# Performance work log

Hardware: AMD Instinct MI355X
Metric: run time of the kernel (lower is better)

Reference implementation:

```python
import jax, jax.numpy as jnp
import numpy as np

HEADS = 16
DIM_HEAD = 64
SCALE = DIM_HEAD ** -0.5


def setup_inputs() -> dict:
    key = jax.random.key(0)
    ks = jax.random.split(key, 6)
    d = 1024
    x = jax.random.normal(ks[0], (4, 2048, d), dtype=jnp.float32)
    s = d ** -0.5
    Wq = jax.random.normal(ks[1], (d, d), dtype=jnp.float32) * s
    Wk = jax.random.normal(ks[2], (d, d), dtype=jnp.float32) * s
    Wv = jax.random.normal(ks[3], (d, d), dtype=jnp.float32) * s
    Wo = jax.random.normal(ks[4], (d, d), dtype=jnp.float32) * s
    bo = jnp.zeros((d,), dtype=jnp.float32)
    return {"x": x, "Wq": Wq, "Wk": Wk, "Wv": Wv, "Wo": Wo, "bo": bo}


def reference(x, Wq, Wk, Wv, Wo, bo):
    b, n, _ = x.shape
    h, dh = HEADS, DIM_HEAD
    # projections (bias-free), split heads: b n (h d) -> b h n d
    def split(t):
        return t.reshape(b, n, h, dh).transpose(0, 2, 1, 3)
    q = split(x @ Wq.T)
    k = split(x @ Wk.T)
    v = split(x @ Wv.T)
    # fp32 scores (inputs already fp32; explicit cast mirrors ATTN_PRECISION='fp32')
    sim = jnp.einsum('bhid,bhjd->bhij', q.astype(jnp.float32), k.astype(jnp.float32)) * SCALE
    attn = jax.nn.softmax(sim, axis=-1)
    out = jnp.einsum('bhij,bhjd->bhid', attn, v)
    out = out.transpose(0, 2, 1, 3).reshape(b, n, h * dh)
    return out @ Wo.T + bo
```

## Files before the change

### kernel.cpp

```cpp
#include <hip/hip_runtime.h>

typedef float f32x4 __attribute__((ext_vector_type(4)));
typedef float f32x16 __attribute__((ext_vector_type(16)));
typedef short s16x8 __attribute__((ext_vector_type(8)));
typedef __bf16 bf16x8 __attribute__((ext_vector_type(8)));
typedef unsigned int u32;
typedef unsigned int u32x4 __attribute__((ext_vector_type(4)));
typedef unsigned short u16;

struct __align__(8) us4 { u16 s[4]; };

#define DEVINL static __device__ __forceinline__

DEVINL f32x4 mfma_bf16(s16x8 a, s16x8 b, f32x4 c) {
  return __builtin_amdgcn_mfma_f32_16x16x32_bf16(
      __builtin_bit_cast(bf16x8, a), __builtin_bit_cast(bf16x8, b), c, 0, 0, 0);
}

DEVINL f32x16 mfma32_bf16(s16x8 a, s16x8 b, f32x16 c) {
  return __builtin_amdgcn_mfma_f32_32x32x16_bf16(
      __builtin_bit_cast(bf16x8, a), __builtin_bit_cast(bf16x8, b), c, 0, 0, 0);
}

DEVINL u16 f2bf(float f) {
  __bf16 h = (__bf16)f;
  return __builtin_bit_cast(u16, h);
}

DEVINL u32 pk2(float a, float b) {
  return (u32)f2bf(a) | ((u32)f2bf(b) << 16);
}

DEVINL void pl32swap(u32& a, u32& b) {
  asm volatile("v_permlane32_swap_b32 %0, %1" : "+v"(a), "+v"(b));
}

DEVINL float exp2_fast(float x) {
  float r;
  asm("v_exp_f32 %0, %1" : "=v"(r) : "v"(x));
  return r;
}

#define GLD16(gp, lp)                                                         \
  __builtin_amdgcn_global_load_lds(                                           \
      (const __attribute__((address_space(1))) void*)(gp),                    \
      (__attribute__((address_space(3))) void*)(lp), 16, 0, 0)

#define SCHEDB() __builtin_amdgcn_sched_barrier(0)

#define WAITV(n)                                                              \
  do {                                                                        \
    asm volatile("s_waitcnt vmcnt(" #n ")" ::: "memory");                     \
    SCHEDB();                                                                 \
  } while (0)

#define BARRIER()                                                             \
  do {                                                                        \
    SCHEDB();                                                                 \
    __builtin_amdgcn_s_barrier();                                             \
    SCHEDB();                                                                 \
  } while (0)

#define PIPE_BAR()                                                            \
  do {                                                                        \
    asm volatile("s_waitcnt vmcnt(0)" ::: "memory");                          \
    SCHEDB();                                                                 \
    __builtin_amdgcn_s_barrier();                                             \
    SCHEDB();                                                                 \
  } while (0)

__global__ __launch_bounds__(256) void convert_k(
    const float* __restrict__ x, const float* __restrict__ wq,
    const float* __restrict__ wk, const float* __restrict__ wv,
    const float* __restrict__ wo, u16* __restrict__ xb,
    u16* __restrict__ wqkv, u16* __restrict__ wob) {
  long i = (long)blockIdx.x * 256 + threadIdx.x;
  const float4* s;
  u16* d;
  if (i < 2097152) {
    s = (const float4*)x + i; d = xb + i * 4;
  } else if (i < 2359296) {
    long j = i - 2097152; s = (const float4*)wq + j; d = wqkv + j * 4;
  } else if (i < 2621440) {
    long j = i - 2359296; s = (const float4*)wk + j; d = wqkv + 1048576 + j * 4;
  } else if (i < 2883584) {
    long j = i - 2621440; s = (const float4*)wv + j; d = wqkv + 2097152 + j * 4;
  } else {
    long j = i - 2883584; s = (const float4*)wo + j; d = wob + j * 4;
  }
  float4 v = *s;
  us4 w;
  w.s[0] = f2bf(v.x); w.s[1] = f2bf(v.y); w.s[2] = f2bf(v.z); w.s[3] = f2bf(v.w);
  *(us4*)d = w;
}

template <int MODE>
__global__ __launch_bounds__(256, 2) void gemm_bt(
    const u16* __restrict__ A, const u16* __restrict__ B,
    u16* __restrict__ oq, u16* __restrict__ ok, u16* __restrict__ ovt,
    float* __restrict__ oc, const float* __restrict__ bias) {
  __shared__ __align__(16) u16 lA[2][128 * 64];
  __shared__ __align__(16) u16 lB[2][128 * 64];
  const int t = threadIdx.x;
  const int wave = t >> 6, lane = t & 63, g = lane >> 4, c = lane & 15;
  const int bm = blockIdx.y, bn = blockIdx.x;
  const int wr = wave >> 1, wc = wave & 1;
  f32x4 acc[4][4] = {};

  const int srow = t >> 3, sch = t & 7;
  const int sgc = (sch ^ (srow & 7)) * 8;
  const u16* abase = A + ((long)bm * 128 + srow) * 1024 + sgc;
  const u16* bbase = B + ((long)bn * 128 + srow) * 1024 + sgc;

  auto stage = [&](int kk, int bi) {
#pragma unroll
    for (int i = 0; i < 4; ++i) {
      GLD16(abase + i * 32 * 1024 + kk, lA[bi] + (i * 256 + wave * 64) * 8);
      GLD16(bbase + i * 32 * 1024 + kk, lB[bi] + (i * 256 + wave * 64) * 8);
    }
  };

  auto compute = [&](int bi) {
#pragma unroll
    for (int k2 = 0; k2 < 2; ++k2) {
      s16x8 af[4], bfr[4];
#pragma unroll
      for (int m = 0; m < 4; ++m) {
        int r = wr * 64 + m * 16 + c;
        af[m] = *(const s16x8*)&lA[bi][r * 64 + (((k2 * 4 + g) ^ (r & 7)) * 8)];
      }
#pragma unroll
      for (int n = 0; n < 4; ++n) {
        int r = wc * 64 + n * 16 + c;
        bfr[n] = *(const s16x8*)&lB[bi][r * 64 + (((k2 * 4 + g) ^ (r & 7)) * 8)];
      }
#pragma unroll
      for (int m = 0; m < 4; ++m)
#pragma unroll
        for (int n = 0; n < 4; ++n)
          acc[m][n] = mfma_bf16(af[m], bfr[n], acc[m][n]);
    }
  };

  stage(0, 0);
  PIPE_BAR();
#pragma unroll 2
  for (int k = 0; k < 15; ++k) {
    stage((k + 1) * 64, (k + 1) & 1);
    compute(k & 1);
    PIPE_BAR();
  }
  compute(1);

  if (MODE == 0) {
    const float SQ = 0.18033688011112042f;
#pragma unroll
    for (int n = 0; n < 4; ++n) {
      int colb = bn * 128 + wc * 64 + n * 16;
      int tsel = colb >> 10;
      int f = colb & 1023;
      int h = f >> 6, d0 = f & 63;
#pragma unroll
      for (int m = 0; m < 4; ++m) {
        int row = bm * 128 + wr * 64 + m * 16 + g * 4;
        int b = row >> 11, nn = row & 2047;
        if (tsel == 0) {
          long base = ((long)(b * 16 + h) * 2048 + nn) * 64 + d0 + c;
#pragma unroll
          for (int j = 0; j < 4; ++j)
            oq[base + (long)j * 64] = f2bf(acc[m][n][j] * SQ);
        } else if (tsel == 1) {
          long base = ((long)(b * 16 + h) * 2048 + nn) * 64 + d0 + c;
#pragma unroll
          for (int j = 0; j < 4; ++j)
            ok[base + (long)j * 64] = f2bf(acc[m][n][j]);
        } else {
          us4 w;
#pragma unroll
          for (int j = 0; j < 4; ++j) w.s[j] = f2bf(acc[m][n][j]);
          *(us4*)&ovt[((long)(b * 16 + h) * 64 + d0 + c) * 2048 + nn] = w;
        }
      }
    }
  } else {
#pragma unroll
    for (int n = 0; n < 4; ++n) {
      int col = bn * 128 + wc * 64 + n * 16 + c;
      float bv = bias[col];
#pragma unroll
      for (int m = 0; m < 4; ++m) {
        int row = bm * 128 + wr * 64 + m * 16 + g * 4;
#pragma unroll
        for (int j = 0; j < 4; ++j)
          oc[(long)(row + j) * 1024 + col] = acc[m][n][j] + bv;
      }
    }
  }
}

__global__ __launch_bounds__(256, 4) void flash_attn(
    const u16* __restrict__ q, const u16* __restrict__ k,
    const u16* __restrict__ vt, u16* __restrict__ ao) {
  __shared__ __align__(16) u16 lds[20480];
  u16* const Kb[3] = {lds, lds + 4096, lds + 8192};
  u16* const Vb[2] = {lds + 12288, lds + 16384};
  const int t = threadIdx.x;
  const int wave = t >> 6, lane = t & 63;
  const int lc = lane & 31, hi = lane >> 5, x7 = lc & 7;
  const int wg = blockIdx.x;
  const int bh = wg & 63, qt = wg >> 6;

  const u16* kb = k + (long)bh * (2048 * 64);
  const u16* vb = vt + (long)bh * (64 * 2048);

  const int srow = t >> 3, sch = t & 7;
  const int sgc = (sch ^ (srow & 7)) * 8;
  const u16* kp = kb + srow * 64 + sgc;
  const u16* vp = vb + srow * 2048 + sgc;

  auto stageK = [&](u16* kd) {
    GLD16(kp, kd + wave * 512);
    GLD16(kp + 2048, kd + 2048 + wave * 512);
    kp += 4096;
  };
  auto stageV = [&](u16* vd) {
    GLD16(vp, vd + wave * 512);
    GLD16(vp + 65536, vd + 2048 + wave * 512);
    vp += 64;
  };

  const u16* qp =
      q + ((long)bh * 2048 + qt * 128 + wave * 32 + lc) * 64 + hi * 8;
  s16x8 bq[4];
#pragma unroll
  for (int kd = 0; kd < 4; ++kd) bq[kd] = *(const s16x8*)(qp + kd * 16);

  float ls = 0.f;
  f32x16 o[2] = {};

  auto qkt = [&](const u16* kB, f32x16 (&st)[2]) {
    __builtin_amdgcn_s_setprio(1);
#pragma unroll
    for (int ks = 0; ks < 2; ++ks)
#pragma unroll
      for (int kd = 0; kd < 4; ++kd) {
        s16x8 ak =
            *(const s16x8*)&kB[(ks * 32 + lc) * 64 + (((kd * 2 + hi) ^ x7) * 8)];
        st[ks] = mfma32_bf16(ak, bq[kd], st[ks]);
      }
    __builtin_amdgcn_s_setprio(0);
  };

  auto softmax = [&](f32x16 (&st)[2]) {
    float ps = 0.f;
#pragma unroll
    for (int ks = 0; ks < 2; ++ks)
#pragma unroll
      for (int i = 0; i < 16; ++i) {
        float p = exp2_fast(st[ks][i]);
        st[ks][i] = p;
        ps += p;
      }
    ps += __shfl_xor(ps, 32);
    ls += ps;
  };

  auto pv = [&](const u16* vB, f32x16 (&st)[2]) {
    __builtin_amdgcn_s_setprio(1);
#pragma unroll
    for (int ks2 = 0; ks2 < 4; ++ks2) {
      const f32x16& P = st[ks2 >> 1];
      const int b0 = (ks2 & 1) * 8;
      u32 A0 = pk2(P[b0 + 0], P[b0 + 1]);
      u32 B0 = pk2(P[b0 + 2], P[b0 + 3]);
      u32 A1 = pk2(P[b0 + 4], P[b0 + 5]);
      u32 B1 = pk2(P[b0 + 6], P[b0 + 7]);
      pl32swap(A0, A1);
      pl32swap(B0, B1);
      u32x4 pw;
      pw[0] = A0; pw[1] = B0; pw[2] = A1; pw[3] = B1;
      s16x8 bp = __builtin_bit_cast(s16x8, pw);
#pragma unroll
      for (int do2 = 0; do2 < 2; ++do2) {
        s16x8 av = *(const s16x8*)&vB[(do2 * 32 + lc) * 64 +
                                      (((ks2 * 2 + hi) ^ x7) * 8)];
        o[do2] = mfma32_bf16(av, bp, o[do2]);
      }
    }
    __builtin_amdgcn_s_setprio(0);
  };

  stageV(Vb[0]);
  stageK(Kb[0]);
  stageK(Kb[1]);
  WAITV(2);
  BARRIER();

  u16 *kcur = Kb[0], *knext = Kb[1], *kthird = Kb[2];
  u16 *vcur = Vb[0], *vother = Vb[1];

#pragma unroll 6
  for (int t2 = 0; t2 < 30; ++t2) {
    stageV(vother);
    stageK(kthird);
    f32x16 st[2] = {};
    qkt(kcur, st);
    softmax(st);
    pv(vcur, st);
    WAITV(2);
    BARRIER();
    u16* tmp = kcur;
    kcur = knext; knext = kthird; kthird = tmp;
    tmp = vcur; vcur = vother; vother = tmp;
  }
  {
    stageV(vother);
    f32x16 st[2] = {};
    qkt(kcur, st);
    softmax(st);
    pv(vcur, st);
    WAITV(0);
    BARRIER();
  }
  {
    f32x16 st[2] = {};
    qkt(knext, st);
    softmax(st);
    pv(vother, st);
  }

  int b = bh >> 4, h = bh & 15;
  u16* ob = ao + ((long)b * 2048 + qt * 128 + wave * 32 + lc) * 1024 + h * 64 +
            hi * 4;
  float inv = 1.0f / ls;
#pragma unroll
  for (int do2 = 0; do2 < 2; ++do2)
#pragma unroll
    for (int tq = 0; tq < 4; ++tq) {
      us4 w;
#pragma unroll
      for (int j = 0; j < 4; ++j) w.s[j] = f2bf(o[do2][tq * 4 + j] * inv);
      *(us4*)&ob[do2 * 32 + tq * 8] = w;
    }
}

extern "C" void kernel_launch(void* const* d_in, const int* in_sizes, int n_in,
                              void* d_out, int out_size, void* d_ws, size_t ws_size,
                              hipStream_t stream) {
  const float* x = (const float*)d_in[0];
  const float* wq = (const float*)d_in[1];
  const float* wk = (const float*)d_in[2];
  const float* wv = (const float*)d_in[3];
  const float* wo = (const float*)d_in[4];
  const float* bo = (const float*)d_in[5];
  char* ws = (char*)d_ws;
  u16* xb   = (u16*)(ws);
  u16* wqkv = (u16*)(ws + (16l << 20));
  u16* wob  = (u16*)(ws + (22l << 20));
  u16* qb   = (u16*)(ws + (24l << 20));
  u16* kbuf = (u16*)(ws + (40l << 20));
  u16* vtb  = (u16*)(ws + (56l << 20));
  u16* aob  = (u16*)(ws + (72l << 20));
  float* out = (float*)d_out;

  convert_k<<<12288, 256, 0, stream>>>(x, wq, wk, wv, wo, xb, wqkv, wob);
  gemm_bt<0><<<dim3(24, 64), 256, 0, stream>>>(xb, wqkv, qb, kbuf, vtb,
                                               nullptr, nullptr);
  flash_attn<<<1024, 256, 0, stream>>>(qb, kbuf, vtb, aob);
  gemm_bt<1><<<dim3(8, 64), 256, 0, stream>>>(aob, wob, nullptr, nullptr,
                                              nullptr, out, bo);
}
```

Measured before the change: 186.4 us.

## Remap GEMM blocks across XCDs and use single-buffered LDS staging

Replaces the 2D GEMM grid with a 1D grid whose block index is remapped so neighbouring output tiles land on the same XCD, aiming for better L2 reuse. It also drops the double-buffered LDS prefetch pipeline in favour of a simple load-sync-compute loop with one buffer, halving LDS use. This trades lost load/compute overlap for possibly higher occupancy and locality.

```diff
diff --git a/kernel.cpp b/kernel.cpp
--- a/kernel.cpp
+++ b/kernel.cpp
@@ -56,14 +56,6 @@
 
 #define BARRIER()                                                             \
   do {                                                                        \
-    SCHEDB();                                                                 \
-    __builtin_amdgcn_s_barrier();                                             \
-    SCHEDB();                                                                 \
-  } while (0)
-
-#define PIPE_BAR()                                                            \
-  do {                                                                        \
-    asm volatile("s_waitcnt vmcnt(0)" ::: "memory");                          \
     SCHEDB();                                                                 \
     __builtin_amdgcn_s_barrier();                                             \
     SCHEDB();                                                                 \
@@ -99,40 +91,43 @@
     const u16* __restrict__ A, const u16* __restrict__ B,
     u16* __restrict__ oq, u16* __restrict__ ok, u16* __restrict__ ovt,
     float* __restrict__ oc, const float* __restrict__ bias) {
-  __shared__ __align__(16) u16 lA[2][128 * 64];
-  __shared__ __align__(16) u16 lB[2][128 * 64];
+  __shared__ __align__(16) u16 lA[128 * 64];
+  __shared__ __align__(16) u16 lB[128 * 64];
   const int t = threadIdx.x;
   const int wave = t >> 6, lane = t & 63, g = lane >> 4, c = lane & 15;
-  const int bm = blockIdx.y, bn = blockIdx.x;
+  const int NBN = (MODE == 0) ? 24 : 8;
+  const int wg = blockIdx.x;
+  const int cpx = gridDim.x >> 3;
+  const int wgp = (wg & 7) * cpx + (wg >> 3);
+  const int bm = wgp / NBN, bn = wgp % NBN;
   const int wr = wave >> 1, wc = wave & 1;
   f32x4 acc[4][4] = {};
-
-  const int srow = t >> 3, sch = t & 7;
-  const int sgc = (sch ^ (srow & 7)) * 8;
-  const u16* abase = A + ((long)bm * 128 + srow) * 1024 + sgc;
-  const u16* bbase = B + ((long)bn * 128 + srow) * 1024 + sgc;
-
-  auto stage = [&](int kk, int bi) {
+  const long arow0 = (long)bm * 128;
+  const long brow0 = (long)bn * 128;
+
+  for (int kk = 0; kk < 1024; kk += 64) {
+    __syncthreads();
 #pragma unroll
     for (int i = 0; i < 4; ++i) {
-      GLD16(abase + i * 32 * 1024 + kk, lA[bi] + (i * 256 + wave * 64) * 8);
-      GLD16(bbase + i * 32 * 1024 + kk, lB[bi] + (i * 256 + wave * 64) * 8);
-    }
-  };
-
-  auto compute = [&](int bi) {
+      int s = i * 256 + t;
+      int row = s >> 3, ch = s & 7;
+      int gc = (ch ^ (row & 7)) * 8;
+      GLD16(A + (arow0 + row) * 1024 + kk + gc, lA + (i * 256 + wave * 64) * 8);
+      GLD16(B + (brow0 + row) * 1024 + kk + gc, lB + (i * 256 + wave * 64) * 8);
+    }
+    __syncthreads();
 #pragma unroll
     for (int k2 = 0; k2 < 2; ++k2) {
       s16x8 af[4], bfr[4];
 #pragma unroll
       for (int m = 0; m < 4; ++m) {
         int r = wr * 64 + m * 16 + c;
-        af[m] = *(const s16x8*)&lA[bi][r * 64 + (((k2 * 4 + g) ^ (r & 7)) * 8)];
+        af[m] = *(const s16x8*)&lA[r * 64 + (((k2 * 4 + g) ^ (r & 7)) * 8)];
       }
 #pragma unroll
       for (int n = 0; n < 4; ++n) {
         int r = wc * 64 + n * 16 + c;
-        bfr[n] = *(const s16x8*)&lB[bi][r * 64 + (((k2 * 4 + g) ^ (r & 7)) * 8)];
+        bfr[n] = *(const s16x8*)&lB[r * 64 + (((k2 * 4 + g) ^ (r & 7)) * 8)];
       }
 #pragma unroll
       for (int m = 0; m < 4; ++m)
@@ -140,17 +135,7 @@
         for (int n = 0; n < 4; ++n)
           acc[m][n] = mfma_bf16(af[m], bfr[n], acc[m][n]);
     }
-  };
-
-  stage(0, 0);
-  PIPE_BAR();
-#pragma unroll 2
-  for (int k = 0; k < 15; ++k) {
-    stage((k + 1) * 64, (k + 1) & 1);
-    compute(k & 1);
-    PIPE_BAR();
-  }
-  compute(1);
+  }
 
   if (MODE == 0) {
     const float SQ = 0.18033688011112042f;
@@ -364,9 +349,9 @@
   float* out = (float*)d_out;
 
   convert_k<<<12288, 256, 0, stream>>>(x, wq, wk, wv, wo, xb, wqkv, wob);
-  gemm_bt<0><<<dim3(24, 64), 256, 0, stream>>>(xb, wqkv, qb, kbuf, vtb,
-                                               nullptr, nullptr);
+  gemm_bt<0><<<1536, 256, 0, stream>>>(xb, wqkv, qb, kbuf, vtb,
+                                       nullptr, nullptr);
   flash_attn<<<1024, 256, 0, stream>>>(qb, kbuf, vtb, aob);
-  gemm_bt<1><<<dim3(8, 64), 256, 0, stream>>>(aob, wob, nullptr, nullptr,
-                                              nullptr, out, bo);
-}
+  gemm_bt<1><<<512, 256, 0, stream>>>(aob, wob, nullptr, nullptr,
+                                      nullptr, out, bo);
+}
```

New measurement: 174.9 us. -6.2%, faster.
